# Kernel tuning notes

Measured on AMD Instinct MI355X. Metric: run time of the kernel, lower is better.

## Reference

```python
import jax, jax.numpy as jnp
import numpy as np

B, N, D_IN, H, L, NH, PE, DEG, OUT = 8, 1024, 128, 256, 4, 8, 8, 16, 1
BN = B * N
E = BN * DEG
DH = H // NH
EPS = 1e-5


def _gelu(x):
    return jax.nn.gelu(x, approximate=False)  # torch nn.GELU default (erf)


def _bn(x, g, b):
    # BatchNorm1d in training mode: batch mean / biased variance over node dim
    m = x.mean(axis=0)
    v = x.var(axis=0)
    return (x - m) * jax.lax.rsqrt(v + EPS) * g + b


def setup_inputs() -> dict:
    key = jax.random.key(0)
    ks = jax.random.split(key, 30)
    s = 0.05
    x = jax.random.normal(ks[0], (BN, D_IN), jnp.float32)
    # block-diagonal COO adjacency: edges stay within each graph's node block
    base = jnp.repeat(jnp.arange(B, dtype=jnp.int32) * N, N * DEG)
    edge_row = base + jax.random.randint(ks[1], (E,), 0, N, jnp.int32)
    edge_col = base + jax.random.randint(ks[2], (E,), 0, N, jnp.int32)
    edge_val = jax.random.uniform(ks[3], (E,), jnp.float32) / DEG
    batch_pe = jax.random.normal(ks[4], (BN, PE), jnp.float32)
    p = {
        'W_in': jax.random.normal(ks[5], (H, D_IN)) * s,
        'b_in': jnp.zeros((H,)),
        'W_pe': jax.random.normal(ks[6], (H, PE)) * s,
        'b_pe': jnp.zeros((H,)),
        'gcn_W': jax.random.normal(ks[7], (L, H, H)) * s,
        'attn_in_W': jax.random.normal(ks[8], (L, 3 * H, H)) * s,
        'attn_in_b': jnp.zeros((L, 3 * H)),
        'attn_out_W': jax.random.normal(ks[9], (L, H, H)) * s,
        'attn_out_b': jnp.zeros((L, H)),
        'bn_g': jnp.ones((L, 3, H)),
        'bn_b': jnp.zeros((L, 3, H)),
        'ffn_W1': jax.random.normal(ks[10], (L, 4 * H, H)) * s,
        'ffn_b1': jnp.zeros((L, 4 * H)),
        'ffn_W2': jax.random.normal(ks[11], (L, H, 4 * H)) * s,
        'ffn_b2': jnp.zeros((L, H)),
        'head_W1': jax.random.normal(ks[12], (H // 2, H)) * s,
        'head_b1': jnp.zeros((H // 2,)),
        'head_W2': jax.random.normal(ks[13], (OUT, H // 2)) * s,
        'head_b2': jnp.zeros((OUT,)),
    }
    p = {k: v.astype(jnp.float32) for k, v in p.items()}
    return dict(x=x, edge_row=edge_row, edge_col=edge_col, edge_val=edge_val,
                batch_pe=batch_pe, **p)


def reference(x, edge_row, edge_col, edge_val, batch_pe,
              W_in, b_in, W_pe, b_pe,
              gcn_W, attn_in_W, attn_in_b, attn_out_W, attn_out_b,
              bn_g, bn_b, ffn_W1, ffn_b1, ffn_W2, ffn_b2,
              head_W1, head_b1, head_W2, head_b2):
    h = x @ W_in.T + b_in + batch_pe @ W_pe.T + b_pe  # (BN, H)
    scale = 1.0 / jnp.sqrt(jnp.asarray(DH, h.dtype))
    for l in range(L):
        # local GCN: linear -> sparse mm (block-diag COO) -> GELU
        msg = edge_val[:, None] * (h @ gcn_W[l].T)[edge_col]  # (E, H)
        h_local = _gelu(jax.ops.segment_sum(msg, edge_row, num_segments=BN))
        h = _bn(h + h_local, bn_g[l, 0], bn_b[l, 0])
        # global self-attention over each graph's N nodes
        hh = h.reshape(B, N, H)
        qkv = hh @ attn_in_W[l].T + attn_in_b[l]  # (B, N, 3H)
        q, k, v = [t.reshape(B, N, NH, DH) for t in jnp.split(qkv, 3, axis=-1)]
        att = jax.nn.softmax(jnp.einsum('bqhd,bkhd->bhqk', q, k) * scale, axis=-1)
        o = jnp.einsum('bhqk,bkhd->bqhd', att, v).reshape(B, N, H)
        o = (o @ attn_out_W[l].T + attn_out_b[l]).reshape(BN, H)
        h = _bn(h + o, bn_g[l, 1], bn_b[l, 1])
        # FFN
        f = _gelu(h @ ffn_W1[l].T + ffn_b1[l]) @ ffn_W2[l].T + ffn_b2[l]
        h = _bn(h + f, bn_g[l, 2], bn_b[l, 2])
    out = jax.nn.sigmoid(_gelu(h @ head_W1.T + head_b1) @ head_W2.T + head_b2)
    return out
```

## Files before the change

### kernel.cpp

```cpp
#include <hip/hip_runtime.h>
#include <hip/hip_bf16.h>
#include <math.h>

#define BB 8
#define NN 1024
#define BN 8192
#define D_IN 128
#define HH 256
#define LL 4
#define NHD 8
#define DH 32
#define EE 131072
#define EPSV 1e-5f

typedef unsigned short u16;
typedef unsigned int u32;
typedef __attribute__((ext_vector_type(8))) short bf16x8;
typedef __attribute__((ext_vector_type(4))) float f32x4;

__device__ __forceinline__ float gelu_erf(float x) {
    return 0.5f * x * (1.0f + erff(x * 0.70710678118654752f));
}

__device__ __forceinline__ u16 f2bf(float v) {
    __hip_bfloat16 b = __float2bfloat16(v);
    return *reinterpret_cast<u16*>(&b);
}

__device__ __forceinline__ float bf2f(u16 u) {
    u32 x = ((u32)u) << 16;
    return __builtin_bit_cast(float, x);
}

__device__ __forceinline__ u32 pack2bf(float lo, float hi) {
    return ((u32)f2bf(hi) << 16) | (u32)f2bf(lo);
}

__global__ __launch_bounds__(256) void cast_bf16_kernel(const float* __restrict__ in,
                                                        u16* __restrict__ out) {
    int i = blockIdx.x * 256 + threadIdx.x;
    float4 v = ((const float4*)in)[i];
    ushort4 o;
    o.x = f2bf(v.x); o.y = f2bf(v.y); o.z = f2bf(v.z); o.w = f2bf(v.w);
    ((ushort4*)out)[i] = o;
}

__global__ __launch_bounds__(256) void hist_kernel(const int* __restrict__ edge_row,
                                                   int* __restrict__ counts) {
    int e = blockIdx.x * 256 + threadIdx.x;
    atomicAdd(&counts[edge_row[e]], 1);
}

__global__ __launch_bounds__(256) void prefix_kernel(const int* __restrict__ counts,
                                                     int* __restrict__ row_start,
                                                     int* __restrict__ cursor) {
    __shared__ int lds[256];
    int t = threadIdx.x;
    int local[32];
    int s = 0;
#pragma unroll
    for (int i = 0; i < 32; ++i) { local[i] = counts[t * 32 + i]; s += local[i]; }
    lds[t] = s;
    __syncthreads();
    for (int off = 1; off < 256; off <<= 1) {
        int v = (t >= off) ? lds[t - off] : 0;
        __syncthreads();
        lds[t] += v;
        __syncthreads();
    }
    int excl = (t == 0) ? 0 : lds[t - 1];
#pragma unroll
    for (int i = 0; i < 32; ++i) {
        int c = local[i];
        row_start[t * 32 + i] = excl;
        cursor[t * 32 + i] = excl;
        excl += c;
    }
    if (t == 255) row_start[8192] = excl;
}

__global__ __launch_bounds__(256) void scatter_kernel(const int* __restrict__ edge_row,
                                                      int* __restrict__ cursor,
                                                      int* __restrict__ csr_e) {
    int e = blockIdx.x * 256 + threadIdx.x;
    int r = edge_row[e];
    int pos = atomicAdd(&cursor[r], 1);
    csr_e[pos] = e;
}

__global__ __launch_bounds__(256) void gcn_gather_kernel(const float* __restrict__ t1,
                                                         const int* __restrict__ row_start,
                                                         const int* __restrict__ csr_e,
                                                         const int* __restrict__ edge_col,
                                                         const float* __restrict__ edge_val,
                                                         float* __restrict__ outb) {
    int wave = threadIdx.x >> 6;
    int lane = threadIdx.x & 63;
    int r = blockIdx.x * 4 + wave;
    float4 acc = make_float4(0.f, 0.f, 0.f, 0.f);
    int p0 = row_start[r], p1 = row_start[r + 1];
    for (int p = p0; p < p1; ++p) {
        int e = csr_e[p];
        int c = edge_col[e];
        float v = edge_val[e];
        float4 src = *(const float4*)&t1[(size_t)c * HH + lane * 4];
        acc.x += v * src.x; acc.y += v * src.y; acc.z += v * src.z; acc.w += v * src.w;
    }
    float4 g;
    g.x = gelu_erf(acc.x); g.y = gelu_erf(acc.y); g.z = gelu_erf(acc.z); g.w = gelu_erf(acc.w);
    *(float4*)&outb[(size_t)r * HH + lane * 4] = g;
}

__global__ __launch_bounds__(256) void bn_reduce_kernel(float* __restrict__ h,
                                                        const float* __restrict__ add,
                                                        float* __restrict__ psum,
                                                        float* __restrict__ psq) {
    int c = threadIdx.x;
    int chunk = blockIdx.x;
    int r0 = chunk * 32;
    float s = 0.f, q = 0.f;
#pragma unroll 4
    for (int i = 0; i < 32; ++i) {
        int idx = (r0 + i) * HH + c;
        float v = h[idx] + add[idx];
        h[idx] = v;
        s += v; q += v * v;
    }
    psum[chunk * HH + c] = s;
    psq[chunk * HH + c] = q;
}

__global__ __launch_bounds__(256) void bn_finalize_kernel(const float* __restrict__ psum,
                                                          const float* __restrict__ psq,
                                                          const float* __restrict__ g,
                                                          const float* __restrict__ b,
                                                          float* __restrict__ scale,
                                                          float* __restrict__ shift) {
    int c = threadIdx.x;
    float s = 0.f, q = 0.f;
    for (int i = 0; i < 256; ++i) { s += psum[i * HH + c]; q += psq[i * HH + c]; }
    float mean = s * (1.f / 8192.f);
    float var = q * (1.f / 8192.f) - mean * mean;
    float sc = g[c] * rsqrtf(var + EPSV);
    scale[c] = sc;
    shift[c] = b[c] - mean * sc;
}

__global__ __launch_bounds__(256) void bn_apply_kernel(float* __restrict__ h,
                                                       u16* __restrict__ hb,
                                                       const float* __restrict__ scale,
                                                       const float* __restrict__ shift) {
    int i = blockIdx.x * 256 + threadIdx.x;
    float4 v = ((float4*)h)[i];
    int c4 = (i & 63) * 4;
    v.x = v.x * scale[c4 + 0] + shift[c4 + 0];
    v.y = v.y * scale[c4 + 1] + shift[c4 + 1];
    v.z = v.z * scale[c4 + 2] + shift[c4 + 2];
    v.w = v.w * scale[c4 + 3] + shift[c4 + 3];
    ((float4*)h)[i] = v;
    ushort4 o;
    o.x = f2bf(v.x); o.y = f2bf(v.y); o.z = f2bf(v.z); o.w = f2bf(v.w);
    ((ushort4*)hb)[i] = o;
}

#define SWZ(row, c8) ((c8) ^ (((row) & 7) << 3))
template <int EPI, int OUTBF>
__global__ __launch_bounds__(256) void gemm_mfma(const u16* __restrict__ A,
                                                 const u16* __restrict__ W,
                                                 const float* __restrict__ bias,
                                                 void* __restrict__ Cout,
                                                 int M, int K, int N) {
    __shared__ u16 As[128][64];
    __shared__ u16 Ws[64][64];
    int t = threadIdx.x;
    int bm = blockIdx.y * 128, bn = blockIdx.x * 64;
    int wid = t >> 6, lane = t & 63;
    int wr = wid >> 1, wc = wid & 1;
    int lr = lane & 15, lg = lane >> 4;

    f32x4 zero = {0.f, 0.f, 0.f, 0.f};
    f32x4 acc[4][2];
#pragma unroll
    for (int mi = 0; mi < 4; ++mi)
#pragma unroll
        for (int ni = 0; ni < 2; ++ni) acc[mi][ni] = zero;

    int sr = t >> 3;
    int c8 = (t & 7) * 8;

    for (int k0 = 0; k0 < K; k0 += 64) {
        __syncthreads();
#pragma unroll
        for (int p = 0; p < 4; ++p) {
            int row = sr + p * 32;
            const u16* src = A + (size_t)(bm + row) * K + k0 + c8;
            *(int4*)&As[row][SWZ(row, c8)] = *(const int4*)src;
        }
#pragma unroll
        for (int p = 0; p < 2; ++p) {
            int row = sr + p * 32;
            const u16* src = W + (size_t)(bn + row) * K + k0 + c8;
            *(int4*)&Ws[row][SWZ(row, c8)] = *(const int4*)src;
        }
        __syncthreads();
#pragma unroll
        for (int kk = 0; kk < 2; ++kk) {
            bf16x8 af[4], bf[2];
#pragma unroll
            for (int mi = 0; mi < 4; ++mi) {
                int row = wr * 64 + mi * 16 + lr;
                af[mi] = *(const bf16x8*)&As[row][SWZ(row, kk * 32 + lg * 8)];
            }
#pragma unroll
            for (int ni = 0; ni < 2; ++ni) {
                int row = wc * 32 + ni * 16 + lr;
                bf[ni] = *(const bf16x8*)&Ws[row][SWZ(row, kk * 32 + lg * 8)];
            }
#pragma unroll
            for (int mi = 0; mi < 4; ++mi)
#pragma unroll
                for (int ni = 0; ni < 2; ++ni)
                    acc[mi][ni] = __builtin_amdgcn_mfma_f32_16x16x32_bf16(af[mi], bf[ni], acc[mi][ni], 0, 0, 0);
        }
    }

#pragma unroll
    for (int ni = 0; ni < 2; ++ni) {
        int col = bn + wc * 32 + ni * 16 + lr;
        float bj = bias ? bias[col] : 0.f;
#pragma unroll
        for (int mi = 0; mi < 4; ++mi) {
#pragma unroll
            for (int r = 0; r < 4; ++r) {
                int row = bm + wr * 64 + mi * 16 + lg * 4 + r;
                float v = acc[mi][ni][r] + bj;
                if (EPI == 1) v = gelu_erf(v);
                if (OUTBF)
                    ((u16*)Cout)[(size_t)row * N + col] = f2bf(v);
                else
                    ((float*)Cout)[(size_t)row * N + col] = v;
            }
        }
    }
}

__global__ __launch_bounds__(256) void pe_add_kernel(const float* __restrict__ pe,
                                                     const float* __restrict__ Wpe,
                                                     const float* __restrict__ bpe,
                                                     float* __restrict__ h,
                                                     u16* __restrict__ hb) {
    __shared__ float Ws[256][9];
    int t = threadIdx.x;
    for (int i = t; i < 2048; i += 256) Ws[i >> 3][i & 7] = Wpe[i];
    __syncthreads();
    int r = blockIdx.x;
    int c = t;
    float s = bpe[c];
    const float* pr = pe + r * 8;
#pragma unroll
    for (int k = 0; k < 8; ++k) s += pr[k] * Ws[c][k];
    float nv = h[(size_t)r * HH + c] + s;
    h[(size_t)r * HH + c] = nv;
    hb[(size_t)r * HH + c] = f2bf(nv);
}

__global__ __launch_bounds__(256) void attn_mfma_kernel(const u16* __restrict__ qkv,
                                                        u16* __restrict__ o) {
    __shared__ __align__(16) u16 Ks[64][40];
    __shared__ __align__(16) u16 Vt[32][72];
    __shared__ __align__(16) u16 Ot[64][40];
    int bid = blockIdx.x;
    int qt = bid & 15;
    int head = (bid >> 4) & 7;
    int b = bid >> 7;
    int t = threadIdx.x;
    int w = t >> 6, lane = t & 63;
    int lr = lane & 15, lg = lane >> 4;

    bf16x8 qf;
    {
        const u16* qsrc = qkv + (size_t)(b * NN + qt * 64 + w * 16 + lr) * 768 + head * DH + lg * 8;
        bf16x8 raw = *(const bf16x8*)qsrc;
#pragma unroll
        for (int j = 0; j < 8; ++j) {
            float f = bf2f((u16)raw[j]) * 0.17677669529663689f;
            qf[j] = (short)f2bf(f);
        }
    }

    f32x4 zero = {0.f, 0.f, 0.f, 0.f};
    f32x4 oacc[2] = {zero, zero};
    float m = -1e30f, l = 0.f;

    int srow = t >> 2;
    int sc8 = (t & 3) * 8;
    const u16* kvbase = qkv + (size_t)(b * NN) * 768 + 256 + head * DH + sc8;

    int srcA = ((lg & 1) << 5) + lr;
    int srcB = srcA + 16;
    int hi = lg >> 1;

    for (int k0 = 0; k0 < NN; k0 += 64) {
        __syncthreads();
        {
            const u16* src = kvbase + (size_t)(k0 + srow) * 768;
            *(int4*)&Ks[srow][sc8] = *(const int4*)src;
            bf16x8 vv = *(const bf16x8*)(src + 256);
#pragma unroll
            for (int j = 0; j < 8; ++j) Vt[sc8 + j][srow] = (u16)vv[j];
        }
        __syncthreads();

        f32x4 st[4];
#pragma unroll
        for (int kt = 0; kt < 4; ++kt) {
            bf16x8 kf = *(const bf16x8*)&Ks[kt * 16 + lr][lg * 8];
            st[kt] = __builtin_amdgcn_mfma_f32_16x16x32_bf16(kf, qf, zero, 0, 0, 0);
        }

        float tm = -1e30f;
#pragma unroll
        for (int kt = 0; kt < 4; ++kt)
#pragma unroll
            for (int r = 0; r < 4; ++r) tm = fmaxf(tm, st[kt][r]);
        tm = fmaxf(tm, __shfl_xor(tm, 16));
        tm = fmaxf(tm, __shfl_xor(tm, 32));
        float mn = fmaxf(m, tm);
        float corr = __expf(m - mn);
        l *= corr;
#pragma unroll
        for (int dh = 0; dh < 2; ++dh)
#pragma unroll
            for (int r = 0; r < 4; ++r) oacc[dh][r] *= corr;

        float ps = 0.f;
        u32 pw0[4], pw1[4];
#pragma unroll
        for (int kt = 0; kt < 4; ++kt) {
            float p0 = __expf(st[kt][0] - mn);
            float p1 = __expf(st[kt][1] - mn);
            float p2 = __expf(st[kt][2] - mn);
            float p3 = __expf(st[kt][3] - mn);
            ps += (p0 + p1) + (p2 + p3);
            pw0[kt] = pack2bf(p0, p1);
            pw1[kt] = pack2bf(p2, p3);
        }
        ps += __shfl_xor(ps, 16);
        ps += __shfl_xor(ps, 32);
        l += ps;
        m = mn;

#pragma unroll
        for (int c = 0; c < 2; ++c) {
            u32 w0a = (u32)__shfl((int)pw0[c * 2], srcA);
            u32 w0b = (u32)__shfl((int)pw0[c * 2 + 1], srcA);
            u32 w1a = (u32)__shfl((int)pw1[c * 2], srcA);
            u32 w1b = (u32)__shfl((int)pw1[c * 2 + 1], srcA);
            u32 w2a = (u32)__shfl((int)pw0[c * 2], srcB);
            u32 w2b = (u32)__shfl((int)pw0[c * 2 + 1], srcB);
            u32 w3a = (u32)__shfl((int)pw1[c * 2], srcB);
            u32 w3b = (u32)__shfl((int)pw1[c * 2 + 1], srcB);
            union { bf16x8 v; u32 u[4]; } pf;
            pf.u[0] = hi ? w0b : w0a;
            pf.u[1] = hi ? w1b : w1a;
            pf.u[2] = hi ? w2b : w2a;
            pf.u[3] = hi ? w3b : w3a;
#pragma unroll
            for (int dh = 0; dh < 2; ++dh) {
                bf16x8 vf = *(const bf16x8*)&Vt[dh * 16 + lr][c * 32 + lg * 8];
                oacc[dh] = __builtin_amdgcn_mfma_f32_16x16x32_bf16(vf, pf.v, oacc[dh], 0, 0, 0);
            }
        }
    }

    float inv = 1.f / l;
    __syncthreads();
#pragma unroll
    for (int dh = 0; dh < 2; ++dh)
#pragma unroll
        for (int r = 0; r < 4; ++r)
            Ot[w * 16 + lr][dh * 16 + lg * 4 + r] = f2bf(oacc[dh][r] * inv);
    __syncthreads();
    {
        int orow = t >> 2, oc8 = (t & 3) * 8;
        u16* dst = o + (size_t)(b * NN + qt * 64 + orow) * HH + head * DH + oc8;
        *(int4*)dst = *(const int4*)&Ot[orow][oc8];
    }
}

__global__ __launch_bounds__(256) void head2_kernel(const float* __restrict__ g1,
                                                    const float* __restrict__ W2,
                                                    const float* __restrict__ b2,
                                                    float* __restrict__ out) {
    __shared__ float w[128];
    int t = threadIdx.x;
    if (t < 128) w[t] = W2[t];
    __syncthreads();
    int r = blockIdx.x * 256 + t;
    float s = b2[0];
    const float* row = g1 + (size_t)r * 128;
#pragma unroll
    for (int k = 0; k < 128; k += 4) {
        float4 v = *(const float4*)&row[k];
        s += v.x * w[k] + v.y * w[k + 1] + v.z * w[k + 2] + v.w * w[k + 3];
    }
    out[r] = 1.f / (1.f + __expf(-s));
}

extern "C" void kernel_launch(void* const* d_in, const int* in_sizes, int n_in,
                              void* d_out, int out_size, void* d_ws, size_t ws_size,
                              hipStream_t stream) {
    const float* x        = (const float*)d_in[0];
    const int*   edge_row = (const int*)d_in[1];
    const int*   edge_col = (const int*)d_in[2];
    const float* edge_val = (const float*)d_in[3];
    const float* pe       = (const float*)d_in[4];
    const float* W_in     = (const float*)d_in[5];
    const float* b_in     = (const float*)d_in[6];
    const float* W_pe     = (const float*)d_in[7];
    const float* b_pe     = (const float*)d_in[8];
    const float* gcn_W    = (const float*)d_in[9];
    const float* attn_in_W  = (const float*)d_in[10];
    const float* attn_in_b  = (const float*)d_in[11];
    const float* attn_out_W = (const float*)d_in[12];
    const float* attn_out_b = (const float*)d_in[13];
    const float* bn_g     = (const float*)d_in[14];
    const float* bn_b     = (const float*)d_in[15];
    const float* ffn_W1   = (const float*)d_in[16];
    const float* ffn_b1   = (const float*)d_in[17];
    const float* ffn_W2   = (const float*)d_in[18];
    const float* ffn_b2   = (const float*)d_in[19];
    const float* head_W1  = (const float*)d_in[20];
    const float* head_b1  = (const float*)d_in[21];
    const float* head_W2  = (const float*)d_in[22];
    const float* head_b2  = (const float*)d_in[23];
    float* out = (float*)d_out;

    float* w = (float*)d_ws;
    float* h    = w; w += 2097152;
    float* buf1 = w; w += 8388608;
    float* buf2 = w; w += 2097152;
    float* buf3 = w; w += 2097152;
    float* psum = w; w += 65536;
    float* psq  = w; w += 65536;
    float* scale = w; w += 256;
    float* shift = w; w += 256;
    int* counts    = (int*)w; w += 8192;
    int* row_start = (int*)w; w += 8224;
    int* cursor    = (int*)w; w += 8192;
    int* csr_e     = (int*)w; w += 131072;
    u16* hb   = (u16*)w;
    u16* xb   = hb + 2097152;
    u16* aob  = xb + 1048576;
    u16* wbWin = aob + 2097152;
    u16* wbGcn = wbWin + 32768;
    u16* wbAin = wbGcn + 262144;
    u16* wbAout = wbAin + 786432;
    u16* wbF1  = wbAout + 262144;
    u16* wbF2  = wbF1 + 1048576;
    u16* wbH1  = wbF2 + 1048576;
    u16* qkvb = (u16*)buf1;
    u16* midb = (u16*)buf1;

    hipMemsetAsync(counts, 0, 8192 * sizeof(int), stream);
    hist_kernel<<<512, 256, 0, stream>>>(edge_row, counts);
    prefix_kernel<<<1, 256, 0, stream>>>(counts, row_start, cursor);
    scatter_kernel<<<512, 256, 0, stream>>>(edge_row, cursor, csr_e);

    cast_bf16_kernel<<<1024, 256, 0, stream>>>(x, xb);
    cast_bf16_kernel<<<32, 256, 0, stream>>>(W_in, wbWin);
    cast_bf16_kernel<<<256, 256, 0, stream>>>(gcn_W, wbGcn);
    cast_bf16_kernel<<<768, 256, 0, stream>>>(attn_in_W, wbAin);
    cast_bf16_kernel<<<256, 256, 0, stream>>>(attn_out_W, wbAout);
    cast_bf16_kernel<<<1024, 256, 0, stream>>>(ffn_W1, wbF1);
    cast_bf16_kernel<<<1024, 256, 0, stream>>>(ffn_W2, wbF2);
    cast_bf16_kernel<<<32, 256, 0, stream>>>(head_W1, wbH1);

    gemm_mfma<0, 0><<<dim3(4, 64), 256, 0, stream>>>(xb, wbWin, b_in, h, BN, D_IN, HH);
    pe_add_kernel<<<BN, 256, 0, stream>>>(pe, W_pe, b_pe, h, hb);

    for (int l = 0; l < LL; ++l) {
        gemm_mfma<0, 0><<<dim3(4, 64), 256, 0, stream>>>(hb, wbGcn + l * 65536, nullptr, buf1, BN, HH, HH);
        gcn_gather_kernel<<<2048, 256, 0, stream>>>(buf1, row_start, csr_e, edge_col, edge_val, buf2);
        bn_reduce_kernel<<<256, 256, 0, stream>>>(h, buf2, psum, psq);
        bn_finalize_kernel<<<1, 256, 0, stream>>>(psum, psq, bn_g + (l * 3 + 0) * 256, bn_b + (l * 3 + 0) * 256, scale, shift);
        bn_apply_kernel<<<2048, 256, 0, stream>>>(h, hb, scale, shift);

        gemm_mfma<0, 1><<<dim3(12, 64), 256, 0, stream>>>(hb, wbAin + l * 196608, attn_in_b + l * 768, qkvb, BN, HH, 768);
        attn_mfma_kernel<<<1024, 256, 0, stream>>>(qkvb, aob);
        gemm_mfma<0, 0><<<dim3(4, 64), 256, 0, stream>>>(aob, wbAout + l * 65536, attn_out_b + l * 256, buf3, BN, HH, HH);
        bn_reduce_kernel<<<256, 256, 0, stream>>>(h, buf3, psum, psq);
        bn_finalize_kernel<<<1, 256, 0, stream>>>(psum, psq, bn_g + (l * 3 + 1) * 256, bn_b + (l * 3 + 1) * 256, scale, shift);
        bn_apply_kernel<<<2048, 256, 0, stream>>>(h, hb, scale, shift);

        gemm_mfma<1, 1><<<dim3(16, 64), 256, 0, stream>>>(hb, wbF1 + l * 262144, ffn_b1 + l * 1024, midb, BN, HH, 1024);
        gemm_mfma<0, 0><<<dim3(4, 64), 256, 0, stream>>>(midb, wbF2 + l * 262144, ffn_b2 + l * 256, buf2, BN, 1024, HH);
        bn_reduce_kernel<<<256, 256, 0, stream>>>(h, buf2, psum, psq);
        bn_finalize_kernel<<<1, 256, 0, stream>>>(psum, psq, bn_g + (l * 3 + 2) * 256, bn_b + (l * 3 + 2) * 256, scale, shift);
        bn_apply_kernel<<<2048, 256, 0, stream>>>(h, hb, scale, shift);
    }

    gemm_mfma<1, 0><<<dim3(2, 64), 256, 0, stream>>>(hb, wbH1, head_b1, buf1, BN, HH, 128);
    head2_kernel<<<32, 256, 0, stream>>>(buf1, head_W2, head_b2, out);
}
```

Before: 962.7 us.

## Batch weight casts, bf16 GCN gather, parallel BN finalize, wider GEMM tiles, pre-transposed V

Merges the eight cast launches into one multi-segment kernel. The GCN linear output is now stored as bf16 so the gather reads half the bytes. BN finalize is spread over 16 blocks with an LDS reduction instead of one serial block. A new 128x128-tile GEMM is used for the QKV and FFN1 projections. A separate kernel transposes V once so attention loads V rows contiguously instead of scatter-writing a transpose into LDS. The costs are an extra launch and buffer for vT, and bf16 rounding of the GCN intermediate.

```diff
diff --git a/kernel.cpp b/kernel.cpp
--- a/kernel.cpp
+++ b/kernel.cpp
@@ -36,13 +36,25 @@
     return ((u32)f2bf(hi) << 16) | (u32)f2bf(lo);
 }
 
-__global__ __launch_bounds__(256) void cast_bf16_kernel(const float* __restrict__ in,
-                                                        u16* __restrict__ out) {
-    int i = blockIdx.x * 256 + threadIdx.x;
-    float4 v = ((const float4*)in)[i];
+__global__ __launch_bounds__(256) void cast_all_kernel(
+        const float* s0, const float* s1, const float* s2, const float* s3,
+        const float* s4, const float* s5, const float* s6, const float* s7,
+        u16* d0, u16* d1, u16* d2, u16* d3, u16* d4, u16* d5, u16* d6, u16* d7) {
+    int blk = blockIdx.x;
+    const float* s; u16* d; int base;
+    if      (blk < 1024) { s = s0; d = d0; base = 0; }
+    else if (blk < 1056) { s = s1; d = d1; base = 1024; }
+    else if (blk < 1312) { s = s2; d = d2; base = 1056; }
+    else if (blk < 2080) { s = s3; d = d3; base = 1312; }
+    else if (blk < 2336) { s = s4; d = d4; base = 2080; }
+    else if (blk < 3360) { s = s5; d = d5; base = 2336; }
+    else if (blk < 4384) { s = s6; d = d6; base = 3360; }
+    else                 { s = s7; d = d7; base = 4384; }
+    int i = (blk - base) * 256 + threadIdx.x;
+    float4 v = ((const float4*)s)[i];
     ushort4 o;
     o.x = f2bf(v.x); o.y = f2bf(v.y); o.z = f2bf(v.z); o.w = f2bf(v.w);
-    ((ushort4*)out)[i] = o;
+    ((ushort4*)d)[i] = o;
 }
 
 __global__ __launch_bounds__(256) void hist_kernel(const int* __restrict__ edge_row,
@@ -88,7 +100,7 @@
     csr_e[pos] = e;
 }
 
-__global__ __launch_bounds__(256) void gcn_gather_kernel(const float* __restrict__ t1,
+__global__ __launch_bounds__(256) void gcn_gather_kernel(const u16* __restrict__ t1b,
                                                          const int* __restrict__ row_start,
                                                          const int* __restrict__ csr_e,
                                                          const int* __restrict__ edge_col,
@@ -97,17 +109,18 @@
     int wave = threadIdx.x >> 6;
     int lane = threadIdx.x & 63;
     int r = blockIdx.x * 4 + wave;
-    float4 acc = make_float4(0.f, 0.f, 0.f, 0.f);
+    float a0 = 0.f, a1 = 0.f, a2 = 0.f, a3 = 0.f;
     int p0 = row_start[r], p1 = row_start[r + 1];
     for (int p = p0; p < p1; ++p) {
         int e = csr_e[p];
         int c = edge_col[e];
         float v = edge_val[e];
-        float4 src = *(const float4*)&t1[(size_t)c * HH + lane * 4];
-        acc.x += v * src.x; acc.y += v * src.y; acc.z += v * src.z; acc.w += v * src.w;
+        ushort4 sv = *(const ushort4*)&t1b[(size_t)c * HH + lane * 4];
+        a0 += v * bf2f(sv.x); a1 += v * bf2f(sv.y);
+        a2 += v * bf2f(sv.z); a3 += v * bf2f(sv.w);
     }
     float4 g;
-    g.x = gelu_erf(acc.x); g.y = gelu_erf(acc.y); g.z = gelu_erf(acc.z); g.w = gelu_erf(acc.w);
+    g.x = gelu_erf(a0); g.y = gelu_erf(a1); g.z = gelu_erf(a2); g.w = gelu_erf(a3);
     *(float4*)&outb[(size_t)r * HH + lane * 4] = g;
 }
 
@@ -136,14 +149,30 @@
                                                           const float* __restrict__ b,
                                                           float* __restrict__ scale,
                                                           float* __restrict__ shift) {
-    int c = threadIdx.x;
+    __shared__ float ls[16][17], lq[16][17];
+    int t = threadIdx.x;
+    int cl = t & 15, grp = t >> 4;
+    int c = blockIdx.x * 16 + cl;
     float s = 0.f, q = 0.f;
-    for (int i = 0; i < 256; ++i) { s += psum[i * HH + c]; q += psq[i * HH + c]; }
-    float mean = s * (1.f / 8192.f);
-    float var = q * (1.f / 8192.f) - mean * mean;
-    float sc = g[c] * rsqrtf(var + EPSV);
-    scale[c] = sc;
-    shift[c] = b[c] - mean * sc;
+#pragma unroll
+    for (int i = 0; i < 16; ++i) {
+        int chunk = grp * 16 + i;
+        s += psum[chunk * HH + c];
+        q += psq[chunk * HH + c];
+    }
+    ls[grp][cl] = s; lq[grp][cl] = q;
+    __syncthreads();
+    if (t < 16) {
+        float ss = 0.f, qq = 0.f;
+#pragma unroll
+        for (int gg = 0; gg < 16; ++gg) { ss += ls[gg][t]; qq += lq[gg][t]; }
+        int ch = blockIdx.x * 16 + t;
+        float mean = ss * (1.f / 8192.f);
+        float var = qq * (1.f / 8192.f) - mean * mean;
+        float sc = g[ch] * rsqrtf(var + EPSV);
+        scale[ch] = sc;
+        shift[ch] = b[ch] - mean * sc;
+    }
 }
 
 __global__ __launch_bounds__(256) void bn_apply_kernel(float* __restrict__ h,
@@ -244,6 +273,82 @@
     }
 }
 
+template <int EPI, int OUTBF>
+__global__ __launch_bounds__(256) void gemm_mfma2(const u16* __restrict__ A,
+                                                  const u16* __restrict__ W,
+                                                  const float* __restrict__ bias,
+                                                  void* __restrict__ Cout,
+                                                  int M, int K, int N) {
+    __shared__ u16 As[128][64];
+    __shared__ u16 Ws[128][64];
+    int t = threadIdx.x;
+    int bm = blockIdx.y * 128, bn = blockIdx.x * 128;
+    int wid = t >> 6, lane = t & 63;
+    int wr = wid >> 1, wc = wid & 1;
+    int lr = lane & 15, lg = lane >> 4;
+
+    f32x4 zero = {0.f, 0.f, 0.f, 0.f};
+    f32x4 acc[4][4];
+#pragma unroll
+    for (int mi = 0; mi < 4; ++mi)
+#pragma unroll
+        for (int ni = 0; ni < 4; ++ni) acc[mi][ni] = zero;
+
+    int sr = t >> 3;
+    int c8 = (t & 7) * 8;
+
+    for (int k0 = 0; k0 < K; k0 += 64) {
+        __syncthreads();
+#pragma unroll
+        for (int p = 0; p < 4; ++p) {
+            int row = sr + p * 32;
+            const u16* srcA = A + (size_t)(bm + row) * K + k0 + c8;
+            *(int4*)&As[row][SWZ(row, c8)] = *(const int4*)srcA;
+            const u16* srcW = W + (size_t)(bn + row) * K + k0 + c8;
+            *(int4*)&Ws[row][SWZ(row, c8)] = *(const int4*)srcW;
+        }
+        __syncthreads();
+#pragma unroll
+        for (int kk = 0; kk < 2; ++kk) {
+            bf16x8 af[4], bf[4];
+#pragma unroll
+            for (int mi = 0; mi < 4; ++mi) {
+                int row = wr * 64 + mi * 16 + lr;
+                af[mi] = *(const bf16x8*)&As[row][SWZ(row, kk * 32 + lg * 8)];
+            }
+#pragma unroll
+            for (int ni = 0; ni < 4; ++ni) {
+                int row = wc * 64 + ni * 16 + lr;
+                bf[ni] = *(const bf16x8*)&Ws[row][SWZ(row, kk * 32 + lg * 8)];
+            }
+#pragma unroll
+            for (int mi = 0; mi < 4; ++mi)
+#pragma unroll
+                for (int ni = 0; ni < 4; ++ni)
+                    acc[mi][ni] = __builtin_amdgcn_mfma_f32_16x16x32_bf16(af[mi], bf[ni], acc[mi][ni], 0, 0, 0);
+        }
+    }
+
+#pragma unroll
+    for (int ni = 0; ni < 4; ++ni) {
+        int col = bn + wc * 64 + ni * 16 + lr;
+        float bj = bias ? bias[col] : 0.f;
+#pragma unroll
+        for (int mi = 0; mi < 4; ++mi) {
+#pragma unroll
+            for (int r = 0; r < 4; ++r) {
+                int row = bm + wr * 64 + mi * 16 + lg * 4 + r;
+                float v = acc[mi][ni][r] + bj;
+                if (EPI == 1) v = gelu_erf(v);
+                if (OUTBF)
+                    ((u16*)Cout)[(size_t)row * N + col] = f2bf(v);
+                else
+                    ((float*)Cout)[(size_t)row * N + col] = v;
+            }
+        }
+    }
+}
+
 __global__ __launch_bounds__(256) void pe_add_kernel(const float* __restrict__ pe,
                                                      const float* __restrict__ Wpe,
                                                      const float* __restrict__ bpe,
@@ -264,7 +369,32 @@
     hb[(size_t)r * HH + c] = f2bf(nv);
 }
 
+__global__ __launch_bounds__(256) void vtrans_kernel(const u16* __restrict__ qkv,
+                                                     u16* __restrict__ vT) {
+    __shared__ u16 Ls[64][64];
+    int bid = blockIdx.x;
+    int kt = bid & 15;
+    int head = (bid >> 4) & 7;
+    int b = bid >> 7;
+    int t = threadIdx.x;
+    int key_l = t >> 2, blkS = t & 3;
+    const u16* src = qkv + (size_t)(b * NN + kt * 64 + key_l) * 768 + 512 + head * DH + blkS * 8;
+    int sb = (blkS ^ (key_l & 7) ^ ((key_l >> 3) & 7)) * 8;
+    *(int4*)&Ls[key_l][sb] = *(const int4*)src;
+    __syncthreads();
+    int d = t >> 3, kc = t & 7;
+    union { u16 a[8]; int4 v; } tmp;
+#pragma unroll
+    for (int j = 0; j < 8; ++j) {
+        int col = (((d >> 3) ^ j ^ kc) << 3) | (d & 7);
+        tmp.a[j] = Ls[kc * 8 + j][col];
+    }
+    u16* dst = vT + (size_t)((b * 8 + head) * 32 + d) * NN + kt * 64 + kc * 8;
+    *(int4*)dst = tmp.v;
+}
+
 __global__ __launch_bounds__(256) void attn_mfma_kernel(const u16* __restrict__ qkv,
+                                                        const u16* __restrict__ vT,
                                                         u16* __restrict__ o) {
     __shared__ __align__(16) u16 Ks[64][40];
     __shared__ __align__(16) u16 Vt[32][72];
@@ -292,9 +422,10 @@
     f32x4 oacc[2] = {zero, zero};
     float m = -1e30f, l = 0.f;
 
-    int srow = t >> 2;
-    int sc8 = (t & 3) * 8;
-    const u16* kvbase = qkv + (size_t)(b * NN) * 768 + 256 + head * DH + sc8;
+    int srow = t >> 2, sc8 = (t & 3) * 8;
+    int vd = t >> 3, vc8 = (t & 7) * 8;
+    const u16* kbase = qkv + (size_t)(b * NN) * 768 + 256 + head * DH + sc8;
+    const u16* vbase = vT + (size_t)((b * 8 + head) * 32 + vd) * NN + vc8;
 
     int srcA = ((lg & 1) << 5) + lr;
     int srcB = srcA + 16;
@@ -302,13 +433,8 @@
 
     for (int k0 = 0; k0 < NN; k0 += 64) {
         __syncthreads();
-        {
-            const u16* src = kvbase + (size_t)(k0 + srow) * 768;
-            *(int4*)&Ks[srow][sc8] = *(const int4*)src;
-            bf16x8 vv = *(const bf16x8*)(src + 256);
-#pragma unroll
-            for (int j = 0; j < 8; ++j) Vt[sc8 + j][srow] = (u16)vv[j];
-        }
+        *(int4*)&Ks[srow][sc8] = *(const int4*)(kbase + (size_t)(k0 + srow) * 768);
+        *(int4*)&Vt[vd][vc8] = *(const int4*)(vbase + k0);
         __syncthreads();
 
         f32x4 st[4];
@@ -459,44 +585,42 @@
     u16* wbF1  = wbAout + 262144;
     u16* wbF2  = wbF1 + 1048576;
     u16* wbH1  = wbF2 + 1048576;
+    u16* t1b  = (u16*)buf1;
     u16* qkvb = (u16*)buf1;
     u16* midb = (u16*)buf1;
+    u16* vT   = (u16*)buf1 + 12582912;
 
     hipMemsetAsync(counts, 0, 8192 * sizeof(int), stream);
     hist_kernel<<<512, 256, 0, stream>>>(edge_row, counts);
     prefix_kernel<<<1, 256, 0, stream>>>(counts, row_start, cursor);
     scatter_kernel<<<512, 256, 0, stream>>>(edge_row, cursor, csr_e);
 
-    cast_bf16_kernel<<<1024, 256, 0, stream>>>(x, xb);
-    cast_bf16_kernel<<<32, 256, 0, stream>>>(W_in, wbWin);
-    cast_bf16_kernel<<<256, 256, 0, stream>>>(gcn_W, wbGcn);
-    cast_bf16_kernel<<<768, 256, 0, stream>>>(attn_in_W, wbAin);
-    cast_bf16_kernel<<<256, 256, 0, stream>>>(attn_out_W, wbAout);
-    cast_bf16_kernel<<<1024, 256, 0, stream>>>(ffn_W1, wbF1);
-    cast_bf16_kernel<<<1024, 256, 0, stream>>>(ffn_W2, wbF2);
-    cast_bf16_kernel<<<32, 256, 0, stream>>>(head_W1, wbH1);
+    cast_all_kernel<<<4416, 256, 0, stream>>>(
+        x, W_in, gcn_W, attn_in_W, attn_out_W, ffn_W1, ffn_W2, head_W1,
+        xb, wbWin, wbGcn, wbAin, wbAout, wbF1, wbF2, wbH1);
 
     gemm_mfma<0, 0><<<dim3(4, 64), 256, 0, stream>>>(xb, wbWin, b_in, h, BN, D_IN, HH);
     pe_add_kernel<<<BN, 256, 0, stream>>>(pe, W_pe, b_pe, h, hb);
 
     for (int l = 0; l < LL; ++l) {
-        gemm_mfma<0, 0><<<dim3(4, 64), 256, 0, stream>>>(hb, wbGcn + l * 65536, nullptr, buf1, BN, HH, HH);
-        gcn_gather_kernel<<<2048, 256, 0, stream>>>(buf1, row_start, csr_e, edge_col, edge_val, buf2);
+        gemm_mfma<0, 1><<<dim3(4, 64), 256, 0, stream>>>(hb, wbGcn + l * 65536, nullptr, t1b, BN, HH, HH);
+        gcn_gather_kernel<<<2048, 256, 0, stream>>>(t1b, row_start, csr_e, edge_col, edge_val, buf2);
         bn_reduce_kernel<<<256, 256, 0, stream>>>(h, buf2, psum, psq);
-        bn_finalize_kernel<<<1, 256, 0, stream>>>(psum, psq, bn_g + (l * 3 + 0) * 256, bn_b + (l * 3 + 0) * 256, scale, shift);
+        bn_finalize_kernel<<<16, 256, 0, stream>>>(psum, psq, bn_g + (l * 3 + 0) * 256, bn_b + (l * 3 + 0) * 256, scale, shift);
         bn_apply_kernel<<<2048, 256, 0, stream>>>(h, hb, scale, shift);
 
-        gemm_mfma<0, 1><<<dim3(12, 64), 256, 0, stream>>>(hb, wbAin + l * 196608, attn_in_b + l * 768, qkvb, BN, HH, 768);
-        attn_mfma_kernel<<<1024, 256, 0, stream>>>(qkvb, aob);
+        gemm_mfma2<0, 1><<<dim3(6, 64), 256, 0, stream>>>(hb, wbAin + l * 196608, attn_in_b + l * 768, qkvb, BN, HH, 768);
+        vtrans_kernel<<<1024, 256, 0, stream>>>(qkvb, vT);
+        attn_mfma_kernel<<<1024, 256, 0, stream>>>(qkvb, vT, aob);
         gemm_mfma<0, 0><<<dim3(4, 64), 256, 0, stream>>>(aob, wbAout + l * 65536, attn_out_b + l * 256, buf3, BN, HH, HH);
         bn_reduce_kernel<<<256, 256, 0, stream>>>(h, buf3, psum, psq);
-        bn_finalize_kernel<<<1, 256, 0, stream>>>(psum, psq, bn_g + (l * 3 + 1) * 256, bn_b + (l * 3 + 1) * 256, scale, shift);
+        bn_finalize_kernel<<<16, 256, 0, stream>>>(psum, psq, bn_g + (l * 3 + 1) * 256, bn_b + (l * 3 + 1) * 256, scale, shift);
         bn_apply_kernel<<<2048, 256, 0, stream>>>(h, hb, scale, shift);
 
-        gemm_mfma<1, 1><<<dim3(16, 64), 256, 0, stream>>>(hb, wbF1 + l * 262144, ffn_b1 + l * 1024, midb, BN, HH, 1024);
+        gemm_mfma2<1, 1><<<dim3(8, 64), 256, 0, stream>>>(hb, wbF1 + l * 262144, ffn_b1 + l * 1024, midb, BN, HH, 1024);
         gemm_mfma<0, 0><<<dim3(4, 64), 256, 0, stream>>>(midb, wbF2 + l * 262144, ffn_b2 + l * 256, buf2, BN, 1024, HH);
         bn_reduce_kernel<<<256, 256, 0, stream>>>(h, buf2, psum, psq);
-        bn_finalize_kernel<<<1, 256, 0, stream>>>(psum, psq, bn_g + (l * 3 + 2) * 256, bn_b + (l * 3 + 2) * 256, scale, shift);
+        bn_finalize_kernel<<<16, 256, 0, stream>>>(psum, psq, bn_g + (l * 3 + 2) * 256, bn_b + (l * 3 + 2) * 256, scale, shift);
         bn_apply_kernel<<<2048, 256, 0, stream>>>(h, hb, scale, shift);
     }
 
```

Result: faster. 844.3 us (-12.3%).
